# Performance work log

Hardware: AMD Instinct MI355X
Metric: run time of the kernel (lower is better)

Reference implementation:

```python
import jax, jax.numpy as jnp
import numpy as np

B, T, C, H = 8, 2048, 1024, 128  # batch, seq (=block_size), n_embd, head_size


def setup_inputs() -> dict:
    key = jax.random.key(0)
    kx, kk, kq, kv = jax.random.split(key, 4)
    x = jax.random.normal(kx, (B, T, C), dtype=jnp.float32)
    # nn.Linear(n_embd, head_size, bias=False) weights, stored as (in, out) for x @ W
    s = 1.0 / np.sqrt(C)
    Wk = jax.random.normal(kk, (C, H), dtype=jnp.float32) * s
    Wq = jax.random.normal(kq, (C, H), dtype=jnp.float32) * s
    Wv = jax.random.normal(kv, (C, H), dtype=jnp.float32) * s
    return {"x": x, "Wk": Wk, "Wq": Wq, "Wv": Wv}


def reference(x, Wk, Wq, Wv):
    # x: [B, T, C]
    Bx, Tx, Cx = x.shape
    k = x @ Wk  # [B, T, H]
    q = x @ Wq  # [B, T, H]
    v = x @ Wv  # [B, T, H]
    # NOTE: source multiplies by C**0.5 (not 1/sqrt), kept faithfully
    wei = jnp.einsum("bth,bsh->bts", q, k) * (Cx ** 0.5)  # [B, T, T]
    causal = jnp.tril(jnp.ones((Tx, Tx), dtype=bool))
    wei = jnp.where(causal, wei, -jnp.inf)
    wei = jax.nn.softmax(wei, axis=-1)
    # dropout omitted (eval-mode reference)
    return wei @ v  # [B, T, H]
```

## Files before the change

### kernel.cpp

```cpp
#include <hip/hip_runtime.h>

constexpr int kB = 8;
constexpr int kT = 2048;
constexpr int kC = 1024;
constexpr int kH = 128;
constexpr int kM = kB * kT;
constexpr size_t kMH = (size_t)kM * kH;
constexpr size_t kWH = (size_t)kC * kH;

typedef __attribute__((ext_vector_type(8))) short bf16x8;
typedef __attribute__((ext_vector_type(4))) float f32x4;


__device__ inline unsigned short f2bf_rne(float f) {
    union { float f; unsigned int u; } x; x.f = f;
    unsigned int r = x.u + 0x7fff + ((x.u >> 16) & 1);
    return (unsigned short)(r >> 16);
}
__device__ inline float bf2f(unsigned short h) {
    union { float f; unsigned int u; } x; x.u = ((unsigned int)h) << 16;
    return x.f;
}
__device__ inline unsigned int pack_hi2(float a, float b) {
    return __builtin_amdgcn_perm(__float_as_uint(b), __float_as_uint(a),
                                 0x07060302u);
}
__device__ inline float hi_part(float v) {
    return __uint_as_float(__float_as_uint(v) & 0xffff0000u);
}
__device__ inline void load_lds16(const unsigned short* g, unsigned short* l) {
    __builtin_amdgcn_global_load_lds(
        (const __attribute__((address_space(1))) unsigned int*)g,
        (__attribute__((address_space(3))) unsigned int*)l, 16, 0, 0);
}
#define RAW_BARRIER()  asm volatile("s_barrier" ::: "memory")
#define WAIT_VM0()     asm volatile("s_waitcnt vmcnt(0)" ::: "memory")

__global__ __launch_bounds__(256) void prep_w(
    const float* __restrict__ Wk, const float* __restrict__ Wq,
    const float* __restrict__ Wv, unsigned short* __restrict__ ws)
{
    const int h = blockIdx.x;
    const int mat = blockIdx.y;
    const float* W = (mat == 0) ? Wq : (mat == 1) ? Wk : Wv;
    unsigned short* hi = ws + 5 * kMH + (size_t)(mat * 2) * kWH;
    unsigned short* lo = hi + kWH;

    const int k0 = threadIdx.x * 4;
    unsigned short hv[4], lv[4];
#pragma unroll
    for (int j = 0; j < 4; ++j) {
        const float f = W[(size_t)(k0 + j) * kH + h];
        hv[j] = f2bf_rne(f);
        lv[j] = f2bf_rne(f - bf2f(hv[j]));
    }
    *(uint2*)&hi[(size_t)h * kC + k0] =
        make_uint2(((unsigned)hv[1] << 16) | hv[0], ((unsigned)hv[3] << 16) | hv[2]);
    *(uint2*)&lo[(size_t)h * kC + k0] =
        make_uint2(((unsigned)lv[1] << 16) | lv[0], ((unsigned)lv[3] << 16) | lv[2]);
}

__global__ __launch_bounds__(256, 2) void qkv_mfma(
    const float* __restrict__ x, unsigned short* __restrict__ ws)
{
    __shared__ __align__(16) unsigned short lds[34816];
    unsigned short* Ahi = lds;
    unsigned short* Alo = lds + 9216;
    unsigned short* Bh  = lds + 18432;
    unsigned short* Bl  = lds + 26624;

    const int idx = blockIdx.x;
    const int tid = threadIdx.x;
    const int w = tid >> 6, lane = tid & 63;
    const int li = lane & 15, quad = lane >> 4;

    if (idx < 256) {
        const int mat = idx & 1;
        const int m0 = (idx >> 1) * 128;
        const unsigned short* wThi = ws + 5 * kMH + (size_t)(mat * 2) * kWH;
        const unsigned short* wTlo = wThi + kWH;
        const int wm = w >> 1, wn = w & 1;

        f32x4 acc[4][4];
#pragma unroll
        for (int i = 0; i < 4; ++i)
#pragma unroll
            for (int j = 0; j < 4; ++j) acc[i][j] = (f32x4){0.f, 0.f, 0.f, 0.f};

        for (int kt = 0; kt < kC; kt += 64) {
            if (kt) __syncthreads();
#pragma unroll
            for (int u = 0; u < 8; ++u) {
                const int f = u * 256 + tid;
                const int row = f >> 4, c4 = (f & 15) * 4;
                const float4 xv =
                    *(const float4*)(x + (size_t)(m0 + row) * kC + kt + c4);
                const float l0 = xv.x - hi_part(xv.x), l1 = xv.y - hi_part(xv.y);
                const float l2 = xv.z - hi_part(xv.z), l3 = xv.w - hi_part(xv.w);
                *(uint2*)&Ahi[row * 72 + c4] =
                    make_uint2(pack_hi2(xv.x, xv.y), pack_hi2(xv.z, xv.w));
                *(uint2*)&Alo[row * 72 + c4] =
                    make_uint2(pack_hi2(l0, l1), pack_hi2(l2, l3));
            }
#pragma unroll
            for (int u = 0; u < 4; ++u) {
                const int f = u * 256 + tid;
                const int row = f >> 3, p = f & 7, g = p ^ (row & 7);
                load_lds16(wThi + (size_t)row * kC + kt + g * 8, Bh + f * 8);
                load_lds16(wTlo + (size_t)row * kC + kt + g * 8, Bl + f * 8);
            }
            __syncthreads();

#pragma unroll
            for (int kc = 0; kc < 2; ++kc) {
                bf16x8 ah[4], al[4];
#pragma unroll
                for (int mt = 0; mt < 4; ++mt) {
                    const int ar = (wm * 64 + mt * 16 + li) * 72 + kc * 32 + quad * 8;
                    ah[mt] = *(const bf16x8*)&Ahi[ar];
                    al[mt] = *(const bf16x8*)&Alo[ar];
                }
#pragma unroll
                for (int nt = 0; nt < 4; ++nt) {
                    const int row = wn * 64 + nt * 16 + li;
                    const int pos = (kc * 4 + quad) ^ (li & 7);
                    const bf16x8 bh = *(const bf16x8*)&Bh[row * 64 + pos * 8];
                    const bf16x8 bl = *(const bf16x8*)&Bl[row * 64 + pos * 8];
#pragma unroll
                    for (int mt = 0; mt < 4; ++mt) {
                        acc[mt][nt] = __builtin_amdgcn_mfma_f32_16x16x32_bf16(ah[mt], bh, acc[mt][nt], 0, 0, 0);
                        acc[mt][nt] = __builtin_amdgcn_mfma_f32_16x16x32_bf16(al[mt], bh, acc[mt][nt], 0, 0, 0);
                        acc[mt][nt] = __builtin_amdgcn_mfma_f32_16x16x32_bf16(ah[mt], bl, acc[mt][nt], 0, 0, 0);
                    }
                }
            }
        }
        unsigned short* hip_ = ws + (size_t)(mat * 2) * kMH;
        unsigned short* lop  = hip_ + kMH;
        const float sc = (mat == 0) ? 32.0f : 1.0f;
#pragma unroll
        for (int mt = 0; mt < 4; ++mt)
#pragma unroll
            for (int nt = 0; nt < 4; ++nt) {
                const int col = wn * 64 + nt * 16 + li;
#pragma unroll
                for (int reg = 0; reg < 4; ++reg) {
                    const int row = m0 + wm * 64 + mt * 16 + quad * 4 + reg;
                    const float v = acc[mt][nt][reg] * sc;
                    hip_[(size_t)row * kH + col] = (unsigned short)(__float_as_uint(v) >> 16);
                    lop[(size_t)row * kH + col] =
                        (unsigned short)(__float_as_uint(v - hi_part(v)) >> 16);
                }
            }
    } else {
        const int m0 = (idx - 256) * 64;
        const unsigned short* wThi = ws + 5 * kMH + (size_t)4 * kWH;
        const int rm = w >> 1, rn = w & 1;

        f32x4 acc[2][4];
#pragma unroll
        for (int i = 0; i < 2; ++i)
#pragma unroll
            for (int j = 0; j < 4; ++j) acc[i][j] = (f32x4){0.f, 0.f, 0.f, 0.f};

        for (int kt = 0; kt < kC; kt += 64) {
            if (kt) __syncthreads();
#pragma unroll
            for (int u = 0; u < 4; ++u) {
                const int f = u * 256 + tid;
                const int row = f >> 4, c4 = (f & 15) * 4;
                const float4 xv =
                    *(const float4*)(x + (size_t)(m0 + row) * kC + kt + c4);
                unsigned short h0 = f2bf_rne(xv.x), h1 = f2bf_rne(xv.y);
                unsigned short h2 = f2bf_rne(xv.z), h3 = f2bf_rne(xv.w);
                *(uint2*)&Ahi[row * 72 + c4] =
                    make_uint2(((unsigned)h1 << 16) | h0, ((unsigned)h3 << 16) | h2);
            }
#pragma unroll
            for (int u = 0; u < 4; ++u) {
                const int f = u * 256 + tid;
                const int row = f >> 3, p = f & 7, g = p ^ (row & 7);
                load_lds16(wThi + (size_t)row * kC + kt + g * 8, Bh + f * 8);
            }
            __syncthreads();

#pragma unroll
            for (int kc = 0; kc < 2; ++kc) {
                bf16x8 a[2];
#pragma unroll
                for (int mt = 0; mt < 2; ++mt)
                    a[mt] = *(const bf16x8*)&Ahi[(rm * 32 + mt * 16 + li) * 72 + kc * 32 + quad * 8];
#pragma unroll
                for (int nt = 0; nt < 4; ++nt) {
                    const int row = rn * 64 + nt * 16 + li;
                    const int pos = (kc * 4 + quad) ^ (li & 7);
                    const bf16x8 bh = *(const bf16x8*)&Bh[row * 64 + pos * 8];
#pragma unroll
                    for (int mt = 0; mt < 2; ++mt)
                        acc[mt][nt] = __builtin_amdgcn_mfma_f32_16x16x32_bf16(a[mt], bh, acc[mt][nt], 0, 0, 0);
                }
            }
        }
        unsigned short* vt = ws + 4 * kMH;
        const int bb = m0 >> 11;
        const int t00 = m0 & (kT - 1);
#pragma unroll
        for (int mt = 0; mt < 2; ++mt)
#pragma unroll
            for (int nt = 0; nt < 4; ++nt) {
                const int h = rn * 64 + nt * 16 + li;
                ushort4 pk;
                pk.x = f2bf_rne(acc[mt][nt][0]);
                pk.y = f2bf_rne(acc[mt][nt][1]);
                pk.z = f2bf_rne(acc[mt][nt][2]);
                pk.w = f2bf_rne(acc[mt][nt][3]);
                const int t0 = t00 + rm * 32 + mt * 16 + quad * 4;
                *(ushort4*)&vt[((size_t)(bb * kH + h)) * kT + t0] = pk;
            }
    }
}

__global__ __launch_bounds__(256, 2) void attn_mfma(
    const unsigned short* __restrict__ ws, float* __restrict__ out)
{
    __shared__ __align__(16) unsigned short Kh0[64 * 128];
    __shared__ __align__(16) unsigned short Kl0[64 * 128];
    __shared__ __align__(16) unsigned short Kh1[64 * 128];
    __shared__ __align__(16) unsigned short Kl1[64 * 128];
    __shared__ __align__(16) unsigned short Ps[4][16][40];
    __shared__ __align__(16) float Ml[2][2][2][16];
    __shared__ __align__(16) unsigned short Os[2][16][136];

    const int tid = threadIdx.x;
    const int w = tid >> 6, lane = tid & 63;
    const int li = lane & 15, quad = lane >> 4;
    const int r = w >> 1, c = w & 1;

    const int idx = blockIdx.x;
    const int b = idx & 7;
    const int j = idx >> 3;
    const int qt = (j < 32) ? j : 95 - j;
    const int i0 = qt * 32;
    const int nj = (qt >> 1) + 1;

    const unsigned short* qhi = ws;
    const unsigned short* qlo = ws + kMH;
    const unsigned short* khi = ws + 2 * kMH;
    const unsigned short* klo = ws + 3 * kMH;
    const unsigned short* vt  = ws + 4 * kMH;

    bf16x8 qh[4], ql[4];
    {
        const size_t qoff = ((size_t)(b * kT + i0 + r * 16 + li)) * kH;
#pragma unroll
        for (int kc = 0; kc < 4; ++kc) {
            qh[kc] = *(const bf16x8*)(qhi + qoff + kc * 32 + quad * 8);
            ql[kc] = *(const bf16x8*)(qlo + qoff + kc * 32 + quad * 8);
        }
    }

    f32x4 o[8];
#pragma unroll
    for (int ht = 0; ht < 8; ++ht) o[ht] = (f32x4){0.f, 0.f, 0.f, 0.f};
    float m_i[4] = {-3.0e38f, -3.0e38f, -3.0e38f, -3.0e38f};
    float l_i[4] = {0.f, 0.f, 0.f, 0.f};

    auto stage = [&](int jtile, unsigned short* Kh, unsigned short* Kl) {
        const size_t kgb = ((size_t)(b * kT + jtile * 64)) * kH;
#pragma unroll
        for (int u = 0; u < 4; ++u) {
            const int f = u * 256 + tid;
            const int row = f >> 4, p = f & 15, g = p ^ (row & 15);
            load_lds16(khi + kgb + row * 128 + g * 8, Kh + f * 8);
            load_lds16(klo + kgb + row * 128 + g * 8, Kl + f * 8);
        }
    };

    auto compute = [&](int jtile, const unsigned short* Kh,
                       const unsigned short* Kl,
                       unsigned short* KhN, unsigned short* KlN) {
        bf16x8 vf[8];
#pragma unroll
        for (int ht = 0; ht < 8; ++ht)
            vf[ht] = *(const bf16x8*)(vt + (size_t)(b * kH + ht * 16 + li) * kT +
                                      jtile * 64 + c * 32 + quad * 8);
        __builtin_amdgcn_sched_barrier(0);
        if (jtile + 1 < nj) stage(jtile + 1, KhN, KlN);

        f32x4 s[2];
        s[0] = (f32x4){0.f, 0.f, 0.f, 0.f};
        s[1] = (f32x4){0.f, 0.f, 0.f, 0.f};
#pragma unroll
        for (int nt = 0; nt < 2; ++nt) {
            const int t = c * 32 + nt * 16 + li;
#pragma unroll
            for (int kc = 0; kc < 4; ++kc) {
                const int pos = (kc * 4 + quad) ^ li;
                const bf16x8 kh = *(const bf16x8*)(Kh + t * 128 + pos * 8);
                const bf16x8 kl = *(const bf16x8*)(Kl + t * 128 + pos * 8);
                s[nt] = __builtin_amdgcn_mfma_f32_16x16x32_bf16(qh[kc], kh, s[nt], 0, 0, 0);
                s[nt] = __builtin_amdgcn_mfma_f32_16x16x32_bf16(ql[kc], kh, s[nt], 0, 0, 0);
                s[nt] = __builtin_amdgcn_mfma_f32_16x16x32_bf16(qh[kc], kl, s[nt], 0, 0, 0);
            }
        }
        if (jtile == nj - 1) {
            const int grow0 = i0 + r * 16 + quad * 4;
            const int gcol0 = jtile * 64 + c * 32 + li;
#pragma unroll
            for (int nt = 0; nt < 2; ++nt)
#pragma unroll
                for (int reg = 0; reg < 4; ++reg)
                    if (gcol0 + nt * 16 > grow0 + reg) s[nt][reg] = -3.0e38f;
        }
        float alpha[4];
#pragma unroll
        for (int reg = 0; reg < 4; ++reg) {
            float mr = fmaxf(s[0][reg], s[1][reg]);
            mr = fmaxf(mr, __shfl_xor(mr, 1));
            mr = fmaxf(mr, __shfl_xor(mr, 2));
            mr = fmaxf(mr, __shfl_xor(mr, 4));
            mr = fmaxf(mr, __shfl_xor(mr, 8));
            const float mn = fmaxf(m_i[reg], mr);
            alpha[reg] = __expf(m_i[reg] - mn);
            m_i[reg] = mn;
            const float p0 = __expf(s[0][reg] - mn);
            const float p1 = __expf(s[1][reg] - mn);
            s[0][reg] = p0; s[1][reg] = p1;
            float rs = p0 + p1;
            rs += __shfl_xor(rs, 1);
            rs += __shfl_xor(rs, 2);
            rs += __shfl_xor(rs, 4);
            rs += __shfl_xor(rs, 8);
            l_i[reg] = l_i[reg] * alpha[reg] + rs;
        }
        const f32x4 av = {alpha[0], alpha[1], alpha[2], alpha[3]};
#pragma unroll
        for (int ht = 0; ht < 8; ++ht) o[ht] *= av;
#pragma unroll
        for (int nt = 0; nt < 2; ++nt)
#pragma unroll
            for (int reg = 0; reg < 4; ++reg)
                Ps[w][quad * 4 + reg][nt * 16 + li] = f2bf_rne(s[nt][reg]);
        const bf16x8 pf = *(const bf16x8*)&Ps[w][li][quad * 8];
#pragma unroll
        for (int ht = 0; ht < 8; ++ht)
            o[ht] = __builtin_amdgcn_mfma_f32_16x16x32_bf16(pf, vf[ht], o[ht], 0, 0, 0);
    };

    stage(0, Kh0, Kl0);
    int jt = 0;
    while (true) {
        WAIT_VM0();
        RAW_BARRIER();
        compute(jt, Kh0, Kl0, Kh1, Kl1);
        if (++jt >= nj) break;
        WAIT_VM0();
        RAW_BARRIER();
        compute(jt, Kh1, Kl1, Kh0, Kl0);
        if (++jt >= nj) break;
    }

    __syncthreads();
#pragma unroll
    for (int reg = 0; reg < 4; ++reg) {
        Ml[r][c][0][quad * 4 + reg] = m_i[reg];
        Ml[r][c][1][quad * 4 + reg] = l_i[reg];
    }
    __syncthreads();
    float a_self[4], linv[4];
#pragma unroll
    for (int reg = 0; reg < 4; ++reg) {
        const float mo = Ml[r][c ^ 1][0][quad * 4 + reg];
        const float lo_ = Ml[r][c ^ 1][1][quad * 4 + reg];
        const float mm = fmaxf(m_i[reg], mo);
        a_self[reg] = __expf(m_i[reg] - mm);
        const float a_oth = __expf(mo - mm);
        linv[reg] = 1.0f / (l_i[reg] * a_self[reg] + lo_ * a_oth);
    }
    if (c == 1) {
#pragma unroll
        for (int ht = 0; ht < 8; ++ht)
#pragma unroll
            for (int reg = 0; reg < 4; ++reg)
                Os[r][quad * 4 + reg][ht * 16 + li] =
                    f2bf_rne(o[ht][reg] * a_self[reg]);
    }
    __syncthreads();
    if (c == 0) {
#pragma unroll
        for (int ht = 0; ht < 8; ++ht)
#pragma unroll
            for (int reg = 0; reg < 4; ++reg) {
                const float v = o[ht][reg] * a_self[reg] +
                                bf2f(Os[r][quad * 4 + reg][ht * 16 + li]);
                out[(size_t)(b * kT + i0 + r * 16 + quad * 4 + reg) * kH +
                    ht * 16 + li] = v * linv[reg];
            }
    }
}

extern "C" void kernel_launch(void* const* d_in, const int* in_sizes, int n_in,
                              void* d_out, int out_size, void* d_ws, size_t ws_size,
                              hipStream_t stream) {
    const float* x  = (const float*)d_in[0];
    const float* Wk = (const float*)d_in[1];
    const float* Wq = (const float*)d_in[2];
    const float* Wv = (const float*)d_in[3];
    unsigned short* ws = (unsigned short*)d_ws;
    float* out = (float*)d_out;

    hipLaunchKernelGGL(prep_w, dim3(128, 3), dim3(256), 0, stream, Wk, Wq, Wv, ws);
    hipLaunchKernelGGL(qkv_mfma, dim3(512), dim3(256), 0, stream, x, ws);
    hipLaunchKernelGGL(attn_mfma, dim3(512), dim3(256), 0, stream,
                       (const unsigned short*)ws, out);
}
```

Before: 216.6 us.

## Retile QKV projection and split attention KV across waves without LDS staging

The QKV projection now uses uniform 64-row tiles with a 32-wide K step over 768 blocks, dropping the separate 128-row path and the two-blocks-per-CU launch bound. Attention no longer double-buffers K tiles through LDS with async loads. Each of the four waves now handles 32 query rows and strides over 32-key chunks, reading K directly from global memory, and the four partial softmax states are merged through an fp32 LDS buffer. This aims to cut LDS traffic and barriers and to balance the causal work across waves, at the cost of uncoalesced, unshared global K reads and more registers per wave.

```diff
diff --git a/kernel.cpp b/kernel.cpp
--- a/kernel.cpp
+++ b/kernel.cpp
@@ -33,8 +33,6 @@
         (const __attribute__((address_space(1))) unsigned int*)g,
         (__attribute__((address_space(3))) unsigned int*)l, 16, 0, 0);
 }
-#define RAW_BARRIER()  asm volatile("s_barrier" ::: "memory")
-#define WAIT_VM0()     asm volatile("s_waitcnt vmcnt(0)" ::: "memory")
 
 __global__ __launch_bounds__(256) void prep_w(
     const float* __restrict__ Wk, const float* __restrict__ Wq,
@@ -60,78 +58,75 @@
         make_uint2(((unsigned)lv[1] << 16) | lv[0], ((unsigned)lv[3] << 16) | lv[2]);
 }
 
-__global__ __launch_bounds__(256, 2) void qkv_mfma(
+__global__ __launch_bounds__(256) void qkv_mfma(
     const float* __restrict__ x, unsigned short* __restrict__ ws)
 {
-    __shared__ __align__(16) unsigned short lds[34816];
-    unsigned short* Ahi = lds;
-    unsigned short* Alo = lds + 9216;
-    unsigned short* Bh  = lds + 18432;
-    unsigned short* Bl  = lds + 26624;
+    __shared__ __align__(16) unsigned short Ah[64][36];
+    __shared__ __align__(16) unsigned short Al[64][36];
+    __shared__ __align__(16) unsigned short Bh[128 * 32];
+    __shared__ __align__(16) unsigned short Bl[128 * 32];
 
     const int idx = blockIdx.x;
+    const int mat = idx >> 8;
+    const int m0 = (idx & 255) * 64;
+    const unsigned short* wThi = ws + 5 * kMH + (size_t)(mat * 2) * kWH;
+    const unsigned short* wTlo = wThi + kWH;
+
     const int tid = threadIdx.x;
     const int w = tid >> 6, lane = tid & 63;
     const int li = lane & 15, quad = lane >> 4;
-
-    if (idx < 256) {
-        const int mat = idx & 1;
-        const int m0 = (idx >> 1) * 128;
-        const unsigned short* wThi = ws + 5 * kMH + (size_t)(mat * 2) * kWH;
-        const unsigned short* wTlo = wThi + kWH;
-        const int wm = w >> 1, wn = w & 1;
-
-        f32x4 acc[4][4];
-#pragma unroll
-        for (int i = 0; i < 4; ++i)
-#pragma unroll
-            for (int j = 0; j < 4; ++j) acc[i][j] = (f32x4){0.f, 0.f, 0.f, 0.f};
-
-        for (int kt = 0; kt < kC; kt += 64) {
+    const int wm = w >> 1, wn = w & 1;
+
+    const int ar = tid >> 2;
+    const int ac = (tid & 3) * 8;
+
+    f32x4 acc[2][4];
+#pragma unroll
+    for (int i = 0; i < 2; ++i)
+#pragma unroll
+        for (int j = 0; j < 4; ++j) acc[i][j] = (f32x4){0.f, 0.f, 0.f, 0.f};
+
+    if (mat <= 1) {
+        for (int kt = 0; kt < kC; kt += 32) {
             if (kt) __syncthreads();
-#pragma unroll
-            for (int u = 0; u < 8; ++u) {
+            {
+                const float4 x0 = *(const float4*)(x + (size_t)(m0 + ar) * kC + kt + ac);
+                const float4 x1 = *(const float4*)(x + (size_t)(m0 + ar) * kC + kt + ac + 4);
+                *(uint2*)&Ah[ar][ac] = make_uint2(pack_hi2(x0.x, x0.y), pack_hi2(x0.z, x0.w));
+                *(uint2*)&Ah[ar][ac + 4] = make_uint2(pack_hi2(x1.x, x1.y), pack_hi2(x1.z, x1.w));
+                const float l0 = x0.x - hi_part(x0.x), l1 = x0.y - hi_part(x0.y);
+                const float l2 = x0.z - hi_part(x0.z), l3 = x0.w - hi_part(x0.w);
+                const float l4 = x1.x - hi_part(x1.x), l5 = x1.y - hi_part(x1.y);
+                const float l6 = x1.z - hi_part(x1.z), l7 = x1.w - hi_part(x1.w);
+                *(uint2*)&Al[ar][ac] = make_uint2(pack_hi2(l0, l1), pack_hi2(l2, l3));
+                *(uint2*)&Al[ar][ac + 4] = make_uint2(pack_hi2(l4, l5), pack_hi2(l6, l7));
+            }
+#pragma unroll
+            for (int u = 0; u < 2; ++u) {
                 const int f = u * 256 + tid;
-                const int row = f >> 4, c4 = (f & 15) * 4;
-                const float4 xv =
-                    *(const float4*)(x + (size_t)(m0 + row) * kC + kt + c4);
-                const float l0 = xv.x - hi_part(xv.x), l1 = xv.y - hi_part(xv.y);
-                const float l2 = xv.z - hi_part(xv.z), l3 = xv.w - hi_part(xv.w);
-                *(uint2*)&Ahi[row * 72 + c4] =
-                    make_uint2(pack_hi2(xv.x, xv.y), pack_hi2(xv.z, xv.w));
-                *(uint2*)&Alo[row * 72 + c4] =
-                    make_uint2(pack_hi2(l0, l1), pack_hi2(l2, l3));
-            }
-#pragma unroll
-            for (int u = 0; u < 4; ++u) {
-                const int f = u * 256 + tid;
-                const int row = f >> 3, p = f & 7, g = p ^ (row & 7);
+                const int row = f >> 2, g = (f & 3) ^ ((f >> 2) & 3);
                 load_lds16(wThi + (size_t)row * kC + kt + g * 8, Bh + f * 8);
                 load_lds16(wTlo + (size_t)row * kC + kt + g * 8, Bl + f * 8);
             }
             __syncthreads();
 
-#pragma unroll
-            for (int kc = 0; kc < 2; ++kc) {
-                bf16x8 ah[4], al[4];
-#pragma unroll
-                for (int mt = 0; mt < 4; ++mt) {
-                    const int ar = (wm * 64 + mt * 16 + li) * 72 + kc * 32 + quad * 8;
-                    ah[mt] = *(const bf16x8*)&Ahi[ar];
-                    al[mt] = *(const bf16x8*)&Alo[ar];
-                }
-#pragma unroll
-                for (int nt = 0; nt < 4; ++nt) {
-                    const int row = wn * 64 + nt * 16 + li;
-                    const int pos = (kc * 4 + quad) ^ (li & 7);
-                    const bf16x8 bh = *(const bf16x8*)&Bh[row * 64 + pos * 8];
-                    const bf16x8 bl = *(const bf16x8*)&Bl[row * 64 + pos * 8];
-#pragma unroll
-                    for (int mt = 0; mt < 4; ++mt) {
-                        acc[mt][nt] = __builtin_amdgcn_mfma_f32_16x16x32_bf16(ah[mt], bh, acc[mt][nt], 0, 0, 0);
-                        acc[mt][nt] = __builtin_amdgcn_mfma_f32_16x16x32_bf16(al[mt], bh, acc[mt][nt], 0, 0, 0);
-                        acc[mt][nt] = __builtin_amdgcn_mfma_f32_16x16x32_bf16(ah[mt], bl, acc[mt][nt], 0, 0, 0);
-                    }
+            bf16x8 ah[2], al[2];
+#pragma unroll
+            for (int mt = 0; mt < 2; ++mt) {
+                ah[mt] = *(const bf16x8*)&Ah[wm * 32 + mt * 16 + li][quad * 8];
+                al[mt] = *(const bf16x8*)&Al[wm * 32 + mt * 16 + li][quad * 8];
+            }
+#pragma unroll
+            for (int nt = 0; nt < 4; ++nt) {
+                const int row = wn * 64 + nt * 16 + li;
+                const int pos = quad ^ (row & 3);
+                const bf16x8 bh = *(const bf16x8*)&Bh[row * 32 + pos * 8];
+                const bf16x8 bl = *(const bf16x8*)&Bl[row * 32 + pos * 8];
+#pragma unroll
+                for (int mt = 0; mt < 2; ++mt) {
+                    acc[mt][nt] = __builtin_amdgcn_mfma_f32_16x16x32_bf16(ah[mt], bh, acc[mt][nt], 0, 0, 0);
+                    acc[mt][nt] = __builtin_amdgcn_mfma_f32_16x16x32_bf16(al[mt], bh, acc[mt][nt], 0, 0, 0);
+                    acc[mt][nt] = __builtin_amdgcn_mfma_f32_16x16x32_bf16(ah[mt], bl, acc[mt][nt], 0, 0, 0);
                 }
             }
         }
@@ -139,13 +134,13 @@
         unsigned short* lop  = hip_ + kMH;
         const float sc = (mat == 0) ? 32.0f : 1.0f;
 #pragma unroll
-        for (int mt = 0; mt < 4; ++mt)
+        for (int mt = 0; mt < 2; ++mt)
 #pragma unroll
             for (int nt = 0; nt < 4; ++nt) {
                 const int col = wn * 64 + nt * 16 + li;
 #pragma unroll
                 for (int reg = 0; reg < 4; ++reg) {
-                    const int row = m0 + wm * 64 + mt * 16 + quad * 4 + reg;
+                    const int row = m0 + wm * 32 + mt * 16 + quad * 4 + reg;
                     const float v = acc[mt][nt][reg] * sc;
                     hip_[(size_t)row * kH + col] = (unsigned short)(__float_as_uint(v) >> 16);
                     lop[(size_t)row * kH + col] =
@@ -153,68 +148,56 @@
                 }
             }
     } else {
-        const int m0 = (idx - 256) * 64;
-        const unsigned short* wThi = ws + 5 * kMH + (size_t)4 * kWH;
-        const int rm = w >> 1, rn = w & 1;
-
-        f32x4 acc[2][4];
-#pragma unroll
-        for (int i = 0; i < 2; ++i)
-#pragma unroll
-            for (int j = 0; j < 4; ++j) acc[i][j] = (f32x4){0.f, 0.f, 0.f, 0.f};
-
-        for (int kt = 0; kt < kC; kt += 64) {
+        for (int kt = 0; kt < kC; kt += 32) {
             if (kt) __syncthreads();
-#pragma unroll
-            for (int u = 0; u < 4; ++u) {
+            {
+                const float4 x0 = *(const float4*)(x + (size_t)(m0 + ar) * kC + kt + ac);
+                const float4 x1 = *(const float4*)(x + (size_t)(m0 + ar) * kC + kt + ac + 4);
+                unsigned short h0 = f2bf_rne(x0.x), h1 = f2bf_rne(x0.y);
+                unsigned short h2 = f2bf_rne(x0.z), h3 = f2bf_rne(x0.w);
+                unsigned short h4 = f2bf_rne(x1.x), h5 = f2bf_rne(x1.y);
+                unsigned short h6 = f2bf_rne(x1.z), h7 = f2bf_rne(x1.w);
+                *(uint2*)&Ah[ar][ac] =
+                    make_uint2(((unsigned)h1 << 16) | h0, ((unsigned)h3 << 16) | h2);
+                *(uint2*)&Ah[ar][ac + 4] =
+                    make_uint2(((unsigned)h5 << 16) | h4, ((unsigned)h7 << 16) | h6);
+            }
+#pragma unroll
+            for (int u = 0; u < 2; ++u) {
                 const int f = u * 256 + tid;
-                const int row = f >> 4, c4 = (f & 15) * 4;
-                const float4 xv =
-                    *(const float4*)(x + (size_t)(m0 + row) * kC + kt + c4);
-                unsigned short h0 = f2bf_rne(xv.x), h1 = f2bf_rne(xv.y);
-                unsigned short h2 = f2bf_rne(xv.z), h3 = f2bf_rne(xv.w);
-                *(uint2*)&Ahi[row * 72 + c4] =
-                    make_uint2(((unsigned)h1 << 16) | h0, ((unsigned)h3 << 16) | h2);
-            }
-#pragma unroll
-            for (int u = 0; u < 4; ++u) {
-                const int f = u * 256 + tid;
-                const int row = f >> 3, p = f & 7, g = p ^ (row & 7);
+                const int row = f >> 2, g = (f & 3) ^ ((f >> 2) & 3);
                 load_lds16(wThi + (size_t)row * kC + kt + g * 8, Bh + f * 8);
             }
             __syncthreads();
 
-#pragma unroll
-            for (int kc = 0; kc < 2; ++kc) {
-                bf16x8 a[2];
+            bf16x8 a[2];
+#pragma unroll
+            for (int mt = 0; mt < 2; ++mt)
+                a[mt] = *(const bf16x8*)&Ah[wm * 32 + mt * 16 + li][quad * 8];
+#pragma unroll
+            for (int nt = 0; nt < 4; ++nt) {
+                const int row = wn * 64 + nt * 16 + li;
+                const int pos = quad ^ (row & 3);
+                const bf16x8 bh = *(const bf16x8*)&Bh[row * 32 + pos * 8];
 #pragma unroll
                 for (int mt = 0; mt < 2; ++mt)
-                    a[mt] = *(const bf16x8*)&Ahi[(rm * 32 + mt * 16 + li) * 72 + kc * 32 + quad * 8];
-#pragma unroll
-                for (int nt = 0; nt < 4; ++nt) {
-                    const int row = rn * 64 + nt * 16 + li;
-                    const int pos = (kc * 4 + quad) ^ (li & 7);
-                    const bf16x8 bh = *(const bf16x8*)&Bh[row * 64 + pos * 8];
-#pragma unroll
-                    for (int mt = 0; mt < 2; ++mt)
-                        acc[mt][nt] = __builtin_amdgcn_mfma_f32_16x16x32_bf16(a[mt], bh, acc[mt][nt], 0, 0, 0);
-                }
+                    acc[mt][nt] = __builtin_amdgcn_mfma_f32_16x16x32_bf16(a[mt], bh, acc[mt][nt], 0, 0, 0);
             }
         }
         unsigned short* vt = ws + 4 * kMH;
         const int bb = m0 >> 11;
-        const int t00 = m0 & (kT - 1);
+        const int t00 = (m0 & (kT - 1)) + wm * 32;
 #pragma unroll
         for (int mt = 0; mt < 2; ++mt)
 #pragma unroll
             for (int nt = 0; nt < 4; ++nt) {
-                const int h = rn * 64 + nt * 16 + li;
+                const int h = wn * 64 + nt * 16 + li;
                 ushort4 pk;
                 pk.x = f2bf_rne(acc[mt][nt][0]);
                 pk.y = f2bf_rne(acc[mt][nt][1]);
                 pk.z = f2bf_rne(acc[mt][nt][2]);
                 pk.w = f2bf_rne(acc[mt][nt][3]);
-                const int t0 = t00 + rm * 32 + mt * 16 + quad * 4;
+                const int t0 = t00 + mt * 16 + quad * 4;
                 *(ushort4*)&vt[((size_t)(bb * kH + h)) * kT + t0] = pk;
             }
     }
@@ -223,25 +206,20 @@
 __global__ __launch_bounds__(256, 2) void attn_mfma(
     const unsigned short* __restrict__ ws, float* __restrict__ out)
 {
-    __shared__ __align__(16) unsigned short Kh0[64 * 128];
-    __shared__ __align__(16) unsigned short Kl0[64 * 128];
-    __shared__ __align__(16) unsigned short Kh1[64 * 128];
-    __shared__ __align__(16) unsigned short Kl1[64 * 128];
-    __shared__ __align__(16) unsigned short Ps[4][16][40];
-    __shared__ __align__(16) float Ml[2][2][2][16];
-    __shared__ __align__(16) unsigned short Os[2][16][136];
+    __shared__ __align__(16) unsigned short Ps[4][2][16][40];
+    __shared__ __align__(16) float Ml[4][32][2];
+    __shared__ __align__(16) float Obuf[3][32][128];
 
     const int tid = threadIdx.x;
     const int w = tid >> 6, lane = tid & 63;
     const int li = lane & 15, quad = lane >> 4;
-    const int r = w >> 1, c = w & 1;
 
     const int idx = blockIdx.x;
     const int b = idx & 7;
     const int j = idx >> 3;
     const int qt = (j < 32) ? j : 95 - j;
     const int i0 = qt * 32;
-    const int nj = (qt >> 1) + 1;
+    const int nc = qt + 1;
 
     const unsigned short* qhi = ws;
     const unsigned short* qlo = ws + kMH;
@@ -249,153 +227,164 @@
     const unsigned short* klo = ws + 3 * kMH;
     const unsigned short* vt  = ws + 4 * kMH;
 
-    bf16x8 qh[4], ql[4];
-    {
-        const size_t qoff = ((size_t)(b * kT + i0 + r * 16 + li)) * kH;
+    bf16x8 qh[2][4], ql[2][4];
+#pragma unroll
+    for (int mi = 0; mi < 2; ++mi) {
+        const size_t qoff = ((size_t)(b * kT + i0 + mi * 16 + li)) * kH;
 #pragma unroll
         for (int kc = 0; kc < 4; ++kc) {
-            qh[kc] = *(const bf16x8*)(qhi + qoff + kc * 32 + quad * 8);
-            ql[kc] = *(const bf16x8*)(qlo + qoff + kc * 32 + quad * 8);
-        }
-    }
-
-    f32x4 o[8];
-#pragma unroll
-    for (int ht = 0; ht < 8; ++ht) o[ht] = (f32x4){0.f, 0.f, 0.f, 0.f};
-    float m_i[4] = {-3.0e38f, -3.0e38f, -3.0e38f, -3.0e38f};
-    float l_i[4] = {0.f, 0.f, 0.f, 0.f};
-
-    auto stage = [&](int jtile, unsigned short* Kh, unsigned short* Kl) {
-        const size_t kgb = ((size_t)(b * kT + jtile * 64)) * kH;
-#pragma unroll
-        for (int u = 0; u < 4; ++u) {
-            const int f = u * 256 + tid;
-            const int row = f >> 4, p = f & 15, g = p ^ (row & 15);
-            load_lds16(khi + kgb + row * 128 + g * 8, Kh + f * 8);
-            load_lds16(klo + kgb + row * 128 + g * 8, Kl + f * 8);
-        }
-    };
-
-    auto compute = [&](int jtile, const unsigned short* Kh,
-                       const unsigned short* Kl,
-                       unsigned short* KhN, unsigned short* KlN) {
+            qh[mi][kc] = *(const bf16x8*)(qhi + qoff + kc * 32 + quad * 8);
+            ql[mi][kc] = *(const bf16x8*)(qlo + qoff + kc * 32 + quad * 8);
+        }
+    }
+
+    f32x4 o[2][8];
+#pragma unroll
+    for (int mi = 0; mi < 2; ++mi)
+#pragma unroll
+        for (int ht = 0; ht < 8; ++ht) o[mi][ht] = (f32x4){0.f, 0.f, 0.f, 0.f};
+    float m_i[2][4], l_i[2][4];
+#pragma unroll
+    for (int mi = 0; mi < 2; ++mi)
+#pragma unroll
+        for (int reg = 0; reg < 4; ++reg) { m_i[mi][reg] = -3.0e38f; l_i[mi][reg] = 0.f; }
+
+    for (int jc = w; jc < nc; jc += 4) {
+        const int t0 = jc * 32;
         bf16x8 vf[8];
 #pragma unroll
         for (int ht = 0; ht < 8; ++ht)
             vf[ht] = *(const bf16x8*)(vt + (size_t)(b * kH + ht * 16 + li) * kT +
-                                      jtile * 64 + c * 32 + quad * 8);
-        __builtin_amdgcn_sched_barrier(0);
-        if (jtile + 1 < nj) stage(jtile + 1, KhN, KlN);
-
-        f32x4 s[2];
-        s[0] = (f32x4){0.f, 0.f, 0.f, 0.f};
-        s[1] = (f32x4){0.f, 0.f, 0.f, 0.f};
-#pragma unroll
-        for (int nt = 0; nt < 2; ++nt) {
-            const int t = c * 32 + nt * 16 + li;
-#pragma unroll
-            for (int kc = 0; kc < 4; ++kc) {
-                const int pos = (kc * 4 + quad) ^ li;
-                const bf16x8 kh = *(const bf16x8*)(Kh + t * 128 + pos * 8);
-                const bf16x8 kl = *(const bf16x8*)(Kl + t * 128 + pos * 8);
-                s[nt] = __builtin_amdgcn_mfma_f32_16x16x32_bf16(qh[kc], kh, s[nt], 0, 0, 0);
-                s[nt] = __builtin_amdgcn_mfma_f32_16x16x32_bf16(ql[kc], kh, s[nt], 0, 0, 0);
-                s[nt] = __builtin_amdgcn_mfma_f32_16x16x32_bf16(qh[kc], kl, s[nt], 0, 0, 0);
-            }
-        }
-        if (jtile == nj - 1) {
-            const int grow0 = i0 + r * 16 + quad * 4;
-            const int gcol0 = jtile * 64 + c * 32 + li;
+                                      t0 + quad * 8);
+        f32x4 s[2][2];
+#pragma unroll
+        for (int mi = 0; mi < 2; ++mi)
+#pragma unroll
+            for (int nt = 0; nt < 2; ++nt) s[mi][nt] = (f32x4){0.f, 0.f, 0.f, 0.f};
+#pragma unroll
+        for (int kc = 0; kc < 4; ++kc) {
+            bf16x8 kh[2], kl[2];
+#pragma unroll
+            for (int nt = 0; nt < 2; ++nt) {
+                const size_t ka =
+                    ((size_t)(b * kT + t0 + nt * 16 + li)) * kH + kc * 32 + quad * 8;
+                kh[nt] = *(const bf16x8*)(khi + ka);
+                kl[nt] = *(const bf16x8*)(klo + ka);
+            }
+#pragma unroll
+            for (int mi = 0; mi < 2; ++mi)
+#pragma unroll
+                for (int nt = 0; nt < 2; ++nt) {
+                    s[mi][nt] = __builtin_amdgcn_mfma_f32_16x16x32_bf16(qh[mi][kc], kh[nt], s[mi][nt], 0, 0, 0);
+                    s[mi][nt] = __builtin_amdgcn_mfma_f32_16x16x32_bf16(ql[mi][kc], kh[nt], s[mi][nt], 0, 0, 0);
+                    s[mi][nt] = __builtin_amdgcn_mfma_f32_16x16x32_bf16(qh[mi][kc], kl[nt], s[mi][nt], 0, 0, 0);
+                }
+        }
+        if (jc == qt) {
+#pragma unroll
+            for (int mi = 0; mi < 2; ++mi) {
+                const int grow0 = i0 + mi * 16 + quad * 4;
+#pragma unroll
+                for (int nt = 0; nt < 2; ++nt) {
+                    const int gcol = t0 + nt * 16 + li;
+#pragma unroll
+                    for (int reg = 0; reg < 4; ++reg)
+                        if (gcol > grow0 + reg) s[mi][nt][reg] = -3.0e38f;
+                }
+            }
+        }
+#pragma unroll
+        for (int mi = 0; mi < 2; ++mi) {
+            float alpha[4];
+#pragma unroll
+            for (int reg = 0; reg < 4; ++reg) {
+                float mr = fmaxf(s[mi][0][reg], s[mi][1][reg]);
+                mr = fmaxf(mr, __shfl_xor(mr, 1));
+                mr = fmaxf(mr, __shfl_xor(mr, 2));
+                mr = fmaxf(mr, __shfl_xor(mr, 4));
+                mr = fmaxf(mr, __shfl_xor(mr, 8));
+                const float mn = fmaxf(m_i[mi][reg], mr);
+                alpha[reg] = __expf(m_i[mi][reg] - mn);
+                m_i[mi][reg] = mn;
+                const float p0 = __expf(s[mi][0][reg] - mn);
+                const float p1 = __expf(s[mi][1][reg] - mn);
+                s[mi][0][reg] = p0; s[mi][1][reg] = p1;
+                float rs = p0 + p1;
+                rs += __shfl_xor(rs, 1);
+                rs += __shfl_xor(rs, 2);
+                rs += __shfl_xor(rs, 4);
+                rs += __shfl_xor(rs, 8);
+                l_i[mi][reg] = l_i[mi][reg] * alpha[reg] + rs;
+            }
+            const f32x4 av = {alpha[0], alpha[1], alpha[2], alpha[3]};
+#pragma unroll
+            for (int ht = 0; ht < 8; ++ht) o[mi][ht] *= av;
 #pragma unroll
             for (int nt = 0; nt < 2; ++nt)
 #pragma unroll
                 for (int reg = 0; reg < 4; ++reg)
-                    if (gcol0 + nt * 16 > grow0 + reg) s[nt][reg] = -3.0e38f;
-        }
-        float alpha[4];
+                    Ps[w][mi][quad * 4 + reg][nt * 16 + li] = f2bf_rne(s[mi][nt][reg]);
+        }
+#pragma unroll
+        for (int mi = 0; mi < 2; ++mi) {
+            const bf16x8 pf = *(const bf16x8*)&Ps[w][mi][li][quad * 8];
+#pragma unroll
+            for (int ht = 0; ht < 8; ++ht)
+                o[mi][ht] = __builtin_amdgcn_mfma_f32_16x16x32_bf16(pf, vf[ht], o[mi][ht], 0, 0, 0);
+        }
+    }
+
+    if (li == 0) {
+#pragma unroll
+        for (int mi = 0; mi < 2; ++mi)
+#pragma unroll
+            for (int reg = 0; reg < 4; ++reg) {
+                Ml[w][mi * 16 + quad * 4 + reg][0] = m_i[mi][reg];
+                Ml[w][mi * 16 + quad * 4 + reg][1] = l_i[mi][reg];
+            }
+    }
+    __syncthreads();
+    float a_self[2][4], linv[2][4];
+#pragma unroll
+    for (int mi = 0; mi < 2; ++mi)
 #pragma unroll
         for (int reg = 0; reg < 4; ++reg) {
-            float mr = fmaxf(s[0][reg], s[1][reg]);
-            mr = fmaxf(mr, __shfl_xor(mr, 1));
-            mr = fmaxf(mr, __shfl_xor(mr, 2));
-            mr = fmaxf(mr, __shfl_xor(mr, 4));
-            mr = fmaxf(mr, __shfl_xor(mr, 8));
-            const float mn = fmaxf(m_i[reg], mr);
-            alpha[reg] = __expf(m_i[reg] - mn);
-            m_i[reg] = mn;
-            const float p0 = __expf(s[0][reg] - mn);
-            const float p1 = __expf(s[1][reg] - mn);
-            s[0][reg] = p0; s[1][reg] = p1;
-            float rs = p0 + p1;
-            rs += __shfl_xor(rs, 1);
-            rs += __shfl_xor(rs, 2);
-            rs += __shfl_xor(rs, 4);
-            rs += __shfl_xor(rs, 8);
-            l_i[reg] = l_i[reg] * alpha[reg] + rs;
-        }
-        const f32x4 av = {alpha[0], alpha[1], alpha[2], alpha[3]};
-#pragma unroll
-        for (int ht = 0; ht < 8; ++ht) o[ht] *= av;
-#pragma unroll
-        for (int nt = 0; nt < 2; ++nt)
-#pragma unroll
-            for (int reg = 0; reg < 4; ++reg)
-                Ps[w][quad * 4 + reg][nt * 16 + li] = f2bf_rne(s[nt][reg]);
-        const bf16x8 pf = *(const bf16x8*)&Ps[w][li][quad * 8];
-#pragma unroll
-        for (int ht = 0; ht < 8; ++ht)
-            o[ht] = __builtin_amdgcn_mfma_f32_16x16x32_bf16(pf, vf[ht], o[ht], 0, 0, 0);
-    };
-
-    stage(0, Kh0, Kl0);
-    int jt = 0;
-    while (true) {
-        WAIT_VM0();
-        RAW_BARRIER();
-        compute(jt, Kh0, Kl0, Kh1, Kl1);
-        if (++jt >= nj) break;
-        WAIT_VM0();
-        RAW_BARRIER();
-        compute(jt, Kh1, Kl1, Kh0, Kl0);
-        if (++jt >= nj) break;
-    }
-
+            const int row = mi * 16 + quad * 4 + reg;
+            const float m0_ = Ml[0][row][0], m1 = Ml[1][row][0];
+            const float m2 = Ml[2][row][0], m3 = Ml[3][row][0];
+            const float ms = fmaxf(fmaxf(m0_, m1), fmaxf(m2, m3));
+            const float L = Ml[0][row][1] * __expf(m0_ - ms) +
+                            Ml[1][row][1] * __expf(m1 - ms) +
+                            Ml[2][row][1] * __expf(m2 - ms) +
+                            Ml[3][row][1] * __expf(m3 - ms);
+            a_self[mi][reg] = __expf(m_i[mi][reg] - ms);
+            linv[mi][reg] = 1.0f / L;
+        }
+    if (w) {
+#pragma unroll
+        for (int mi = 0; mi < 2; ++mi)
+#pragma unroll
+            for (int ht = 0; ht < 8; ++ht)
+#pragma unroll
+                for (int reg = 0; reg < 4; ++reg)
+                    Obuf[w - 1][mi * 16 + quad * 4 + reg][ht * 16 + li] =
+                        o[mi][ht][reg] * a_self[mi][reg];
+    }
     __syncthreads();
-#pragma unroll
-    for (int reg = 0; reg < 4; ++reg) {
-        Ml[r][c][0][quad * 4 + reg] = m_i[reg];
-        Ml[r][c][1][quad * 4 + reg] = l_i[reg];
-    }
-    __syncthreads();
-    float a_self[4], linv[4];
-#pragma unroll
-    for (int reg = 0; reg < 4; ++reg) {
-        const float mo = Ml[r][c ^ 1][0][quad * 4 + reg];
-        const float lo_ = Ml[r][c ^ 1][1][quad * 4 + reg];
-        const float mm = fmaxf(m_i[reg], mo);
-        a_self[reg] = __expf(m_i[reg] - mm);
-        const float a_oth = __expf(mo - mm);
-        linv[reg] = 1.0f / (l_i[reg] * a_self[reg] + lo_ * a_oth);
-    }
-    if (c == 1) {
-#pragma unroll
-        for (int ht = 0; ht < 8; ++ht)
-#pragma unroll
-            for (int reg = 0; reg < 4; ++reg)
-                Os[r][quad * 4 + reg][ht * 16 + li] =
-                    f2bf_rne(o[ht][reg] * a_self[reg]);
-    }
-    __syncthreads();
-    if (c == 0) {
-#pragma unroll
-        for (int ht = 0; ht < 8; ++ht)
-#pragma unroll
-            for (int reg = 0; reg < 4; ++reg) {
-                const float v = o[ht][reg] * a_self[reg] +
-                                bf2f(Os[r][quad * 4 + reg][ht * 16 + li]);
-                out[(size_t)(b * kT + i0 + r * 16 + quad * 4 + reg) * kH +
-                    ht * 16 + li] = v * linv[reg];
-            }
+    if (w == 0) {
+#pragma unroll
+        for (int mi = 0; mi < 2; ++mi)
+#pragma unroll
+            for (int ht = 0; ht < 8; ++ht)
+#pragma unroll
+                for (int reg = 0; reg < 4; ++reg) {
+                    const int row = mi * 16 + quad * 4 + reg;
+                    const int col = ht * 16 + li;
+                    const float v = o[mi][ht][reg] * a_self[mi][reg] +
+                                    Obuf[0][row][col] + Obuf[1][row][col] +
+                                    Obuf[2][row][col];
+                    out[(size_t)(b * kT + i0 + row) * kH + col] = v * linv[mi][reg];
+                }
     }
 }
 
@@ -410,7 +399,7 @@
     float* out = (float*)d_out;
 
     hipLaunchKernelGGL(prep_w, dim3(128, 3), dim3(256), 0, stream, Wk, Wq, Wv, ws);
-    hipLaunchKernelGGL(qkv_mfma, dim3(512), dim3(256), 0, stream, x, ws);
+    hipLaunchKernelGGL(qkv_mfma, dim3(768), dim3(256), 0, stream, x, ws);
     hipLaunchKernelGGL(attn_mfma, dim3(512), dim3(256), 0, stream,
                        (const unsigned short*)ws, out);
 }
```

Result: faster. 199.2 us (-8.0%).
